# Kernel tuning notes

Hardware: AMD Instinct MI355X
Metric: run time of the kernel (lower is better)

The kernel has to match this reference:

```python
import jax, jax.numpy as jnp
import numpy as np

N, E, G, H, D = 30000, 480000, 128, 4, 64
NF, EF, GF, L = 92, 50, 108, 5
EPS = 1e-3  # keras BatchNormalization default epsilon


def _bn(t, g, b, m, v):
    # inference-mode batch norm with running stats
    return (t - m) * jax.lax.rsqrt(v + EPS) * g + b


def _forward(x, edge_attr, global_features,
             node_W, node_b, edge_W, edge_b,
             conv_W, conv_att, conv_bias, conv_bn_g, conv_bn_b, conv_bn_m, conv_bn_v,
             ga_W0, ga_b0, ga_bn0_g, ga_bn0_b, ga_bn0_m, ga_bn0_v,
             ga_W1, ga_b1, ga_bn1_g, ga_bn1_b, ga_bn1_m, ga_bn1_v,
             ga_W2, ga_b2, out_W0, out_b0, out_W1, out_b1,
             edge_index, batch_idx, num_graphs):
    lrelu = lambda t: jax.nn.leaky_relu(t, 0.2)
    row, col = edge_index[0], edge_index[1]
    n = x.shape[0]

    x = lrelu(x @ node_W + node_b)          # [N, D] node embedding
    ea = lrelu(edge_attr @ edge_W + edge_b)  # [E, D] edge embedding

    def conv(xc, p):
        W, att, bias, g, b, m, v = p
        xi = (jnp.concatenate([xc[row], ea], -1) @ W).reshape(-1, H, D)  # [E,H,D]
        xj = (jnp.concatenate([xc[col], ea], -1) @ W).reshape(-1, H, D)
        score = jnp.einsum('ehd,hd->eh', jnp.concatenate([xi, xj], -1), att)
        a = jnp.exp(_bn(lrelu(score), g, b, m, v))            # [E,H]
        norm = jax.ops.segment_sum(a, row, num_segments=n)    # edge softmax denom
        a = a / norm[row]
        msg = xj * a[..., None]                               # [E,H,D]
        # faithful to original: transpose then flat reshape before scatter-add
        msg = jnp.transpose(msg, (1, 0, 2)).reshape(-1, H * D)
        agg = jax.ops.segment_sum(msg, row, num_segments=n)
        out = agg.reshape(n, H, D).mean(axis=1) + bias
        return xc + out, None  # residual connection (done in GATGNN.call)

    x, _ = jax.lax.scan(conv, x, (conv_W, conv_att, conv_bias,
                                  conv_bn_g, conv_bn_b, conv_bn_m, conv_bn_v))

    # global attention pooling
    feat = jnp.concatenate([x, global_features[batch_idx]], -1)  # [N, D+GF]
    h = jax.nn.relu(_bn(feat @ ga_W0 + ga_b0, ga_bn0_g, ga_bn0_b, ga_bn0_m, ga_bn0_v))
    h = jax.nn.relu(_bn(h @ ga_W1 + ga_b1, ga_bn1_g, ga_bn1_b, ga_bn1_m, ga_bn1_v))
    a = jnp.exp(h @ ga_W2 + ga_b2)                               # [N,1]
    norm = jax.ops.segment_sum(a, batch_idx, num_segments=num_graphs)
    a = a / norm[batch_idx]
    pooled = jax.ops.segment_sum(x * a, batch_idx, num_segments=num_graphs)  # [G,D]
    out = jax.nn.relu(pooled @ out_W0 + out_b0) @ out_W1 + out_b1
    return out.squeeze(-1)  # output_dim == 1


def setup_inputs() -> dict:
    key = jax.random.key(0)
    ks = jax.random.split(key, 16)
    s = 0.05
    return {
        'x': jax.random.normal(ks[0], (N, NF), jnp.float32),
        'edge_attr': jax.random.normal(ks[1], (E, EF), jnp.float32),
        'global_features': jax.random.normal(ks[2], (G, GF), jnp.float32),
        'node_W': jax.random.normal(ks[3], (NF, D)) * s, 'node_b': jnp.zeros((D,)),
        'edge_W': jax.random.normal(ks[4], (EF, D)) * s, 'edge_b': jnp.zeros((D,)),
        'conv_W': jax.random.normal(ks[5], (L, 2 * D, H * D)) * s,
        'conv_att': jax.random.normal(ks[6], (L, H, 2 * D)) * s,
        'conv_bias': jnp.zeros((L, D)),
        'conv_bn_g': jnp.ones((L, H)), 'conv_bn_b': jnp.zeros((L, H)),
        'conv_bn_m': jnp.zeros((L, H)), 'conv_bn_v': jnp.ones((L, H)),
        'ga_W0': jax.random.normal(ks[7], (D + GF, D)) * s, 'ga_b0': jnp.zeros((D,)),
        'ga_bn0_g': jnp.ones((D,)), 'ga_bn0_b': jnp.zeros((D,)),
        'ga_bn0_m': jnp.zeros((D,)), 'ga_bn0_v': jnp.ones((D,)),
        'ga_W1': jax.random.normal(ks[8], (D, D)) * s, 'ga_b1': jnp.zeros((D,)),
        'ga_bn1_g': jnp.ones((D,)), 'ga_bn1_b': jnp.zeros((D,)),
        'ga_bn1_m': jnp.zeros((D,)), 'ga_bn1_v': jnp.ones((D,)),
        'ga_W2': jax.random.normal(ks[9], (D, 1)) * s, 'ga_b2': jnp.zeros((1,)),
        'out_W0': jax.random.normal(ks[10], (D, D)) * s, 'out_b0': jnp.zeros((D,)),
        'out_W1': jax.random.normal(ks[11], (D, 1)) * s, 'out_b1': jnp.zeros((1,)),
        'edge_index': jax.random.randint(ks[12], (2, E), 0, N),
        'batch_idx': jnp.sort(jax.random.randint(ks[13], (N,), 0, G)),
        'num_graphs': G,
    }


def reference(x, edge_attr, global_features, node_W, node_b, edge_W, edge_b,
              conv_W, conv_att, conv_bias, conv_bn_g, conv_bn_b, conv_bn_m, conv_bn_v,
              ga_W0, ga_b0, ga_bn0_g, ga_bn0_b, ga_bn0_m, ga_bn0_v,
              ga_W1, ga_b1, ga_bn1_g, ga_bn1_b, ga_bn1_m, ga_bn1_v,
              ga_W2, ga_b2, out_W0, out_b0, out_W1, out_b1,
              edge_index, batch_idx, num_graphs):
    return _forward(x, edge_attr, global_features, node_W, node_b, edge_W, edge_b,
                    conv_W, conv_att, conv_bias, conv_bn_g, conv_bn_b, conv_bn_m, conv_bn_v,
                    ga_W0, ga_b0, ga_bn0_g, ga_bn0_b, ga_bn0_m, ga_bn0_v,
                    ga_W1, ga_b1, ga_bn1_g, ga_bn1_b, ga_bn1_m, ga_bn1_v,
                    ga_W2, ga_b2, out_W0, out_b0, out_W1, out_b1,
                    edge_index, batch_idx, num_graphs)
```

## Files before the change

kernel.cpp:

```cpp
#include <hip/hip_runtime.h>

constexpr int N = 30000, E = 480000, G = 128, H = 4, D = 64;
constexpr int NF = 92, EF = 50, GF = 108, L = 5;
constexpr int EQ = E / 4;
constexpr float EPS = 1e-3f;

__device__ __forceinline__ float lrelu(float t) { return t > 0.f ? t : 0.2f * t; }

__device__ __forceinline__ unsigned short f2bf(float f) {
  unsigned int u = __float_as_uint(f);
  u += 0x7FFFu + ((u >> 16) & 1u);
  return (unsigned short)(u >> 16);
}
__device__ __forceinline__ float bf2f(unsigned short s) {
  return __uint_as_float(((unsigned int)s) << 16);
}

__global__ __launch_bounds__(256) void hist_kernel(const int* __restrict__ row,
                                                   int* __restrict__ deg) {
  int e = blockIdx.x * 256 + threadIdx.x;
  atomicAdd(&deg[row[e]], 1);
}

__global__ __launch_bounds__(1024) void scan_kernel(const int* __restrict__ deg,
                                                    int* __restrict__ start) {
  __shared__ int wsum[16];
  __shared__ int cbase;
  if (threadIdx.x == 0) cbase = 0;
  __syncthreads();
  int lane = threadIdx.x & 63, wave = threadIdx.x >> 6;
  for (int base = 0; base < N; base += 1024) {
    int i = base + (int)threadIdx.x;
    int v = (i < N) ? deg[i] : 0;
    int s = v;
#pragma unroll
    for (int off = 1; off < 64; off <<= 1) { int t = __shfl_up(s, off); if (lane >= off) s += t; }
    if (lane == 63) wsum[wave] = s;
    __syncthreads();
    if (wave == 0 && lane < 16) {
      int w = wsum[lane];
#pragma unroll
      for (int off = 1; off < 16; off <<= 1) { int t = __shfl_up(w, off); if (lane >= off) w += t; }
      wsum[lane] = w;
    }
    __syncthreads();
    int wbase = wave ? wsum[wave - 1] : 0;
    if (i < N) start[i] = cbase + wbase + (s - v);
    __syncthreads();
    if (threadIdx.x == 0) cbase += wsum[15];
    __syncthreads();
  }
  if (threadIdx.x == 0) start[N] = cbase;
}

__global__ __launch_bounds__(256) void fill_kernel(
    const int* __restrict__ row, const int* __restrict__ start, int* __restrict__ cur,
    int* __restrict__ eid_s) {
  int e = blockIdx.x * 256 + threadIdx.x;
  int r = row[e];
  int pos = start[r] + atomicAdd(&cur[r], 1);
  eid_s[pos] = e;
}

template <int K, bool BF16OUT>
__global__ __launch_bounds__(256) void embed7_kernel(
    const float* __restrict__ in, const float* __restrict__ W,
    const float* __restrict__ bias, float* __restrict__ outF,
    unsigned short* __restrict__ outB, int ntiles) {
  constexpr int KP = (K + 3) & ~3;
  constexpr int NL = (16 * K + 255) / 256;
  __shared__ float xs[2][16][KP];
  int tid = threadIdx.x, lane = tid & 63, wave = tid >> 6;
  if (K != KP) {
    for (int f = tid; f < 2 * 16 * KP; f += 256)
      if (f % KP >= K) ((float*)xs)[f] = 0.f;
  }
  float wreg[KP];
#pragma unroll
  for (int k = 0; k < K; k++) wreg[k] = W[k * 64 + lane];
#pragma unroll
  for (int k = K; k < KP; k++) wreg[k] = 0.f;
  float bb = bias[lane];
  float stage[NL];
  int t = blockIdx.x;
  if (t < ntiles) {
#pragma unroll
    for (int i = 0; i < NL; i++) { int f = tid + i * 256; if (f < 16 * K) stage[i] = in[(size_t)t * 16 * K + f]; }
#pragma unroll
    for (int i = 0; i < NL; i++) { int f = tid + i * 256; if (f < 16 * K) xs[0][f / K][f % K] = stage[i]; }
  }
  __syncthreads();
  int cur = 0;
  for (; t < ntiles; t += gridDim.x) {
    int nxt = t + gridDim.x;
    if (nxt < ntiles) {
#pragma unroll
      for (int i = 0; i < NL; i++) { int f = tid + i * 256; if (f < 16 * K) stage[i] = in[(size_t)nxt * 16 * K + f]; }
    }
    float a0 = 0.f, a1 = 0.f, a2 = 0.f, a3 = 0.f;
#pragma unroll
    for (int kc = 0; kc < KP / 4; kc++) {
      float4 x0 = *(const float4*)&xs[cur][wave * 4 + 0][kc * 4];
      float4 x1 = *(const float4*)&xs[cur][wave * 4 + 1][kc * 4];
      float4 x2 = *(const float4*)&xs[cur][wave * 4 + 2][kc * 4];
      float4 x3 = *(const float4*)&xs[cur][wave * 4 + 3][kc * 4];
      float w0 = wreg[kc * 4], w1 = wreg[kc * 4 + 1], w2 = wreg[kc * 4 + 2], w3 = wreg[kc * 4 + 3];
      a0 = fmaf(x0.x, w0, fmaf(x0.y, w1, fmaf(x0.z, w2, fmaf(x0.w, w3, a0))));
      a1 = fmaf(x1.x, w0, fmaf(x1.y, w1, fmaf(x1.z, w2, fmaf(x1.w, w3, a1))));
      a2 = fmaf(x2.x, w0, fmaf(x2.y, w1, fmaf(x2.z, w2, fmaf(x2.w, w3, a2))));
      a3 = fmaf(x3.x, w0, fmaf(x3.y, w1, fmaf(x3.z, w2, fmaf(x3.w, w3, a3))));
    }
    size_t o = ((size_t)t * 16 + wave * 4) * 64 + lane;
    float r0 = lrelu(a0 + bb), r1 = lrelu(a1 + bb), r2 = lrelu(a2 + bb), r3 = lrelu(a3 + bb);
    if (BF16OUT) {
      outB[o] = f2bf(r0); outB[o + 64] = f2bf(r1);
      outB[o + 128] = f2bf(r2); outB[o + 192] = f2bf(r3);
    } else {
      outF[o] = r0; outF[o + 64] = r1; outF[o + 128] = r2; outF[o + 192] = r3;
    }
    if (nxt < ntiles) {
#pragma unroll
      for (int i = 0; i < NL; i++) { int f = tid + i * 256; if (f < 16 * K) xs[cur ^ 1][f / K][f % K] = stage[i]; }
    }
    __syncthreads();
    cur ^= 1;
  }
}

__global__ __launch_bounds__(256) void aes_watt_all_kernel(
    const float* __restrict__ conv_W, const float* __restrict__ conv_att,
    float* __restrict__ AesT, float* __restrict__ WattT) {
  int l = blockIdx.x;
  const float* W = conv_W + (size_t)l * 128 * 256;
  const float* att = conv_att + (size_t)l * H * 128;
  int t = threadIdx.x;
  {
    int h = t >> 6, k = t & 63;
    float acc = 0.f;
    for (int d = 0; d < 64; d++)
      acc = fmaf(W[(64 + k) * 256 + h * 64 + d], att[h * 128 + d] + att[h * 128 + 64 + d], acc);
    AesT[l * 256 + h * 64 + k] = acc;
  }
  for (int idx = t; idx < 512; idx += 256) {
    int hh = idx >> 6, k = idx & 63;
    int h = hh >> 1, ij = hh & 1;
    float acc = 0.f;
    for (int d = 0; d < 64; d++)
      acc = fmaf(W[k * 256 + h * 64 + d], att[h * 128 + ij * 64 + d], acc);
    WattT[l * 512 + idx] = acc;
  }
}

__global__ __launch_bounds__(256) void qs_kernel(
    const unsigned short* __restrict__ ea, const float* __restrict__ AesT,
    float* __restrict__ qsAll) {
  int tid = threadIdx.x;
  int e = blockIdx.x * 16 + (tid >> 4);
  int k4 = tid & 15;
  uint2 raw = *(const uint2*)&ea[(size_t)e * 64 + k4 * 4];
  float e0 = __uint_as_float(raw.x << 16);
  float e1 = __uint_as_float(raw.x & 0xFFFF0000u);
  float e2 = __uint_as_float(raw.y << 16);
  float e3 = __uint_as_float(raw.y & 0xFFFF0000u);
#pragma unroll
  for (int l = 0; l < L; l++) {
    float q0, q1, q2, q3;
    {
      float4 c0 = *(const float4*)&AesT[l * 256 + 0 * 64 + k4 * 4];
      float4 c1 = *(const float4*)&AesT[l * 256 + 1 * 64 + k4 * 4];
      float4 c2 = *(const float4*)&AesT[l * 256 + 2 * 64 + k4 * 4];
      float4 c3 = *(const float4*)&AesT[l * 256 + 3 * 64 + k4 * 4];
      q0 = e0 * c0.x + e1 * c0.y + e2 * c0.z + e3 * c0.w;
      q1 = e0 * c1.x + e1 * c1.y + e2 * c1.z + e3 * c1.w;
      q2 = e0 * c2.x + e1 * c2.y + e2 * c2.z + e3 * c2.w;
      q3 = e0 * c3.x + e1 * c3.y + e2 * c3.z + e3 * c3.w;
    }
#pragma unroll
    for (int off = 1; off < 16; off <<= 1) {
      q0 += __shfl_xor(q0, off); q1 += __shfl_xor(q1, off);
      q2 += __shfl_xor(q2, off); q3 += __shfl_xor(q3, off);
    }
    if (k4 < 4) {
      float qv = (k4 == 0) ? q0 : (k4 == 1) ? q1 : (k4 == 2) ? q2 : q3;
      qsAll[(size_t)l * E * 4 + (size_t)e * 4 + k4] = qv;
    }
  }
}

__global__ __launch_bounds__(256) void xw_kernel(
    const float* __restrict__ xc, const float* __restrict__ W, const float* __restrict__ WattT,
    unsigned short* __restrict__ xWh, float* __restrict__ pi, float* __restrict__ pj) {
  __shared__ float xs[16][64];
  __shared__ float wlT[8][68];
  int tid = threadIdx.x, blk = blockIdx.x, n0 = blk * 16;
  for (int f = tid; f < 1024; f += 256) xs[f >> 6][f & 63] = xc[(size_t)n0 * 64 + f];
  for (int f = tid; f < 512; f += 256) wlT[f >> 6][f & 63] = WattT[f];
  __syncthreads();
  float acc[16];
#pragma unroll
  for (int n = 0; n < 16; n++) acc[n] = 0.f;
#pragma unroll 4
  for (int kc = 0; kc < 16; kc++) {
    float w0 = W[(4 * kc + 0) * 256 + tid];
    float w1 = W[(4 * kc + 1) * 256 + tid];
    float w2 = W[(4 * kc + 2) * 256 + tid];
    float w3 = W[(4 * kc + 3) * 256 + tid];
#pragma unroll
    for (int n = 0; n < 16; n++) {
      float4 xv = *(const float4*)&xs[n][4 * kc];
      acc[n] = fmaf(xv.x, w0, fmaf(xv.y, w1, fmaf(xv.z, w2, fmaf(xv.w, w3, acc[n]))));
    }
  }
  int h = tid >> 6, dd = tid & 63;
#pragma unroll
  for (int n = 0; n < 16; n++)
    xWh[((size_t)h * N + (n0 + n)) * 64 + dd] = f2bf(acc[n]);
  if (tid < 128) {
    int n = tid >> 3, hh = tid & 7;
    float a = 0.f;
#pragma unroll
    for (int kc = 0; kc < 16; kc++) {
      float4 xv = *(const float4*)&xs[n][4 * kc];
      float4 wv = *(const float4*)&wlT[hh][4 * kc];
      a = fmaf(xv.x, wv.x, fmaf(xv.y, wv.y, fmaf(xv.z, wv.z, fmaf(xv.w, wv.w, a))));
    }
    int hq = hh >> 1, ij = hh & 1;
    float* dst = ij ? pj : pi;
    dst[(n0 + n) * 4 + hq] = a;
  }
}

__global__ __launch_bounds__(256) void score2_kernel(
    const float* __restrict__ qs, const float* __restrict__ pi, const float* __restrict__ pj,
    const int* __restrict__ row, const int* __restrict__ col,
    const float* __restrict__ bng, const float* __restrict__ bnb,
    const float* __restrict__ bnm, const float* __restrict__ bnv,
    float* __restrict__ aArr) {
  int e = blockIdx.x * 256 + threadIdx.x;
  int r = row[e], c = col[e];
  float4 q = ((const float4*)qs)[e];
  float4 piv = ((const float4*)pi)[r];
  float4 pjv = ((const float4*)pj)[c];
  float A0 = bng[0] * rsqrtf(bnv[0] + EPS), B0 = bnb[0] - bnm[0] * A0;
  float A1 = bng[1] * rsqrtf(bnv[1] + EPS), B1 = bnb[1] - bnm[1] * A1;
  float A2 = bng[2] * rsqrtf(bnv[2] + EPS), B2 = bnb[2] - bnm[2] * A2;
  float A3 = bng[3] * rsqrtf(bnv[3] + EPS), B3 = bnb[3] - bnm[3] * A3;
  float4 out;
  out.x = expf(lrelu(piv.x + pjv.x + q.x) * A0 + B0);
  out.y = expf(lrelu(piv.y + pjv.y + q.y) * A1 + B1);
  out.z = expf(lrelu(piv.z + pjv.z + q.z) * A2 + B2);
  out.w = expf(lrelu(piv.w + pjv.w + q.w) * A3 + B3);
  ((float4*)aArr)[e] = out;
}

__global__ __launch_bounds__(256) void normsum_kernel(
    const float* __restrict__ aArr, const int* __restrict__ start,
    const int* __restrict__ eid_s, float* __restrict__ inv) {
  int n = blockIdx.x * 256 + threadIdx.x;
  if (n >= N) return;
  int s0 = start[n], s1 = start[n + 1];
  float4 s = {0.f, 0.f, 0.f, 0.f};
  int p = s0;
  for (; p + 4 <= s1; p += 4) {
    int e0 = eid_s[p], e1 = eid_s[p + 1], e2 = eid_s[p + 2], e3 = eid_s[p + 3];
    float4 a0 = ((const float4*)aArr)[e0];
    float4 a1 = ((const float4*)aArr)[e1];
    float4 a2 = ((const float4*)aArr)[e2];
    float4 a3 = ((const float4*)aArr)[e3];
    s.x += (a0.x + a1.x) + (a2.x + a3.x);
    s.y += (a0.y + a1.y) + (a2.y + a3.y);
    s.z += (a0.z + a1.z) + (a2.z + a3.z);
    s.w += (a0.w + a1.w) + (a2.w + a3.w);
  }
  for (; p < s1; p++) {
    float4 a = ((const float4*)aArr)[eid_s[p]];
    s.x += a.x; s.y += a.y; s.z += a.z; s.w += a.w;
  }
  float4 iv;
  if (s1 > s0) { iv.x = 1.f / s.x; iv.y = 1.f / s.y; iv.z = 1.f / s.z; iv.w = 1.f / s.w; }
  else         { iv.x = iv.y = iv.z = iv.w = 0.f; }
  ((float4*)inv)[n] = iv;
}

__global__ __launch_bounds__(256) void zyquad_kernel(
    const float* __restrict__ aArr, const float* __restrict__ invA,
    const unsigned short* __restrict__ ea, const unsigned short* __restrict__ xWh,
    const int* __restrict__ row, const int* __restrict__ col,
    unsigned short* __restrict__ Ybf, unsigned short* __restrict__ Zbf) {
  int q = blockIdx.x * 4 + (threadIdx.x >> 6);
  int lane = threadIdx.x & 63;
  const unsigned short* er = ea + (size_t)q * 256 + lane;
  float e0 = bf2f(er[0]), e1 = bf2f(er[64]), e2 = bf2f(er[128]), e3 = bf2f(er[192]);
  int4 rw = *(const int4*)&row[4 * q];
  int4 cl = *(const int4*)&col[4 * q];
  float4 A0 = ((const float4*)aArr)[4 * q + 0];
  float4 A1 = ((const float4*)aArr)[4 * q + 1];
  float4 A2 = ((const float4*)aArr)[4 * q + 2];
  float4 A3 = ((const float4*)aArr)[4 * q + 3];
  float4 I0 = ((const float4*)invA)[rw.x];
  float4 I1 = ((const float4*)invA)[rw.y];
  float4 I2 = ((const float4*)invA)[rw.z];
  float4 I3 = ((const float4*)invA)[rw.w];
  float c0[4] = {A0.x * I0.x, A0.y * I0.y, A0.z * I0.z, A0.w * I0.w};
  float c1[4] = {A1.x * I1.x, A1.y * I1.y, A1.z * I1.z, A1.w * I1.w};
  float c2[4] = {A2.x * I2.x, A2.y * I2.y, A2.z * I2.z, A2.w * I2.w};
  float c3[4] = {A3.x * I3.x, A3.y * I3.y, A3.z * I3.z, A3.w * I3.w};
#pragma unroll
  for (int h = 0; h < 4; h++) {
    const unsigned short* xw = xWh + (size_t)h * N * 64 + lane;
    float g0 = bf2f(xw[(size_t)cl.x * 64]);
    float g1 = bf2f(xw[(size_t)cl.y * 64]);
    float g2 = bf2f(xw[(size_t)cl.z * 64]);
    float g3 = bf2f(xw[(size_t)cl.w * 64]);
    float y = fmaf(c0[h], e0, fmaf(c1[h], e1, fmaf(c2[h], e2, c3[h] * e3)));
    float z = fmaf(c0[h], g0, fmaf(c1[h], g1, fmaf(c2[h], g2, c3[h] * g3)));
    size_t r = (size_t)h * EQ + q;
    Ybf[r * 64 + lane] = f2bf(y);
    Zbf[r * 64 + lane] = f2bf(z);
  }
}

__global__ __launch_bounds__(256) void scatter2_kernel(
    const unsigned short* __restrict__ Zbf, const unsigned short* __restrict__ Ybf,
    const int* __restrict__ start, const int* __restrict__ eid_s,
    float* __restrict__ out1, float* __restrict__ Bacc) {
  int wave = threadIdx.x >> 6, lane = threadIdx.x & 63;
  int n = blockIdx.x * 4 + wave;
  int s0 = __builtin_amdgcn_readfirstlane(start[n]);
  int s1 = __builtin_amdgcn_readfirstlane(start[n + 1]);
  float m = 0.f;
  float b0 = 0.f, b1 = 0.f, b2 = 0.f, b3 = 0.f;
  int p = s0;
  for (; p + 4 <= s1; p += 4) {
    int r0 = eid_s[p], r1 = eid_s[p + 1], r2 = eid_s[p + 2], r3 = eid_s[p + 3];
    float z0 = bf2f(Zbf[(size_t)r0 * 64 + lane]);
    float z1 = bf2f(Zbf[(size_t)r1 * 64 + lane]);
    float z2 = bf2f(Zbf[(size_t)r2 * 64 + lane]);
    float z3 = bf2f(Zbf[(size_t)r3 * 64 + lane]);
    float y0 = bf2f(Ybf[(size_t)r0 * 64 + lane]);
    float y1 = bf2f(Ybf[(size_t)r1 * 64 + lane]);
    float y2 = bf2f(Ybf[(size_t)r2 * 64 + lane]);
    float y3 = bf2f(Ybf[(size_t)r3 * 64 + lane]);
    m += (z0 + z1) + (z2 + z3);
    int h0 = r0 / EQ, h1 = r1 / EQ, h2 = r2 / EQ, h3 = r3 / EQ;
    if (h0 == 0) b0 += y0; else if (h0 == 1) b1 += y0; else if (h0 == 2) b2 += y0; else b3 += y0;
    if (h1 == 0) b0 += y1; else if (h1 == 1) b1 += y1; else if (h1 == 2) b2 += y1; else b3 += y1;
    if (h2 == 0) b0 += y2; else if (h2 == 1) b1 += y2; else if (h2 == 2) b2 += y2; else b3 += y2;
    if (h3 == 0) b0 += y3; else if (h3 == 1) b1 += y3; else if (h3 == 2) b2 += y3; else b3 += y3;
  }
  for (; p < s1; p++) {
    int r = eid_s[p];
    float z = bf2f(Zbf[(size_t)r * 64 + lane]);
    float y = bf2f(Ybf[(size_t)r * 64 + lane]);
    m += z;
    int h = r / EQ;
    if (h == 0) b0 += y; else if (h == 1) b1 += y; else if (h == 2) b2 += y; else b3 += y;
  }
  out1[(size_t)n * 64 + lane] = m;
  float* Bn = Bacc + (size_t)n * 256 + lane;
  Bn[0] = b0; Bn[64] = b1; Bn[128] = b2; Bn[192] = b3;
}

__global__ __launch_bounds__(256) void finish_kernel(
    const float* __restrict__ out1, const float* __restrict__ Bacc,
    const float* __restrict__ W, const float* __restrict__ bias, float* __restrict__ xc) {
  __shared__ float Bl[16][256];
  int tid = threadIdx.x, blk = blockIdx.x;
  for (int f = tid; f < 4096; f += 256) Bl[f >> 8][f & 255] = Bacc[(size_t)blk * 4096 + f];
  __syncthreads();
  int lane = tid & 63, wave = tid >> 6;
  float a0 = 0.f, a1 = 0.f, a2 = 0.f, a3 = 0.f;
#pragma unroll
  for (int h = 0; h < 4; h++) {
#pragma unroll 4
    for (int kc = 0; kc < 16; kc++) {
      float w0 = W[(64 + 4 * kc + 0) * 256 + h * 64 + lane];
      float w1 = W[(64 + 4 * kc + 1) * 256 + h * 64 + lane];
      float w2 = W[(64 + 4 * kc + 2) * 256 + h * 64 + lane];
      float w3 = W[(64 + 4 * kc + 3) * 256 + h * 64 + lane];
      float4 b0v = *(const float4*)&Bl[wave * 4 + 0][h * 64 + 4 * kc];
      float4 b1v = *(const float4*)&Bl[wave * 4 + 1][h * 64 + 4 * kc];
      float4 b2v = *(const float4*)&Bl[wave * 4 + 2][h * 64 + 4 * kc];
      float4 b3v = *(const float4*)&Bl[wave * 4 + 3][h * 64 + 4 * kc];
      a0 = fmaf(b0v.x, w0, fmaf(b0v.y, w1, fmaf(b0v.z, w2, fmaf(b0v.w, w3, a0))));
      a1 = fmaf(b1v.x, w0, fmaf(b1v.y, w1, fmaf(b1v.z, w2, fmaf(b1v.w, w3, a1))));
      a2 = fmaf(b2v.x, w0, fmaf(b2v.y, w1, fmaf(b2v.z, w2, fmaf(b2v.w, w3, a2))));
      a3 = fmaf(b3v.x, w0, fmaf(b3v.y, w1, fmaf(b3v.z, w2, fmaf(b3v.w, w3, a3))));
    }
  }
  float bb = bias[lane];
  size_t i0 = (size_t)(blk * 16 + wave * 4) * 64 + lane;
  xc[i0]       += bb + 0.25f * (out1[i0] + a0);
  xc[i0 + 64]  += bb + 0.25f * (out1[i0 + 64] + a1);
  xc[i0 + 128] += bb + 0.25f * (out1[i0 + 128] + a2);
  xc[i0 + 192] += bb + 0.25f * (out1[i0 + 192] + a3);
}

__global__ __launch_bounds__(256) void gacontrib_kernel(
    const float* __restrict__ gfeat, const float* __restrict__ W0,
    const float* __restrict__ b0, float* __restrict__ gc) {
  __shared__ float gs[16][GF];
  int tid = threadIdx.x, blk = blockIdx.x;
  int lane = tid & 63, wave = tid >> 6;
  for (int f = tid; f < 16 * GF; f += 256) gs[f / GF][f % GF] = gfeat[(size_t)blk * 16 * GF + f];
  float wreg[GF];
#pragma unroll
  for (int k = 0; k < GF; k++) wreg[k] = W0[(64 + k) * 64 + lane];
  __syncthreads();
  float a0 = 0.f, a1 = 0.f, a2 = 0.f, a3 = 0.f;
#pragma unroll
  for (int kc = 0; kc < GF / 4; kc++) {
    float4 x0 = *(const float4*)&gs[wave * 4 + 0][kc * 4];
    float4 x1 = *(const float4*)&gs[wave * 4 + 1][kc * 4];
    float4 x2 = *(const float4*)&gs[wave * 4 + 2][kc * 4];
    float4 x3 = *(const float4*)&gs[wave * 4 + 3][kc * 4];
    float w0 = wreg[kc * 4], w1 = wreg[kc * 4 + 1], w2 = wreg[kc * 4 + 2], w3 = wreg[kc * 4 + 3];
    a0 = fmaf(x0.x, w0, fmaf(x0.y, w1, fmaf(x0.z, w2, fmaf(x0.w, w3, a0))));
    a1 = fmaf(x1.x, w0, fmaf(x1.y, w1, fmaf(x1.z, w2, fmaf(x1.w, w3, a1))));
    a2 = fmaf(x2.x, w0, fmaf(x2.y, w1, fmaf(x2.z, w2, fmaf(x2.w, w3, a2))));
    a3 = fmaf(x3.x, w0, fmaf(x3.y, w1, fmaf(x3.z, w2, fmaf(x3.w, w3, a3))));
  }
  float bb = b0[lane];
  size_t o = ((size_t)blk * 16 + wave * 4) * 64 + lane;
  gc[o]       = a0 + bb;
  gc[o + 64]  = a1 + bb;
  gc[o + 128] = a2 + bb;
  gc[o + 192] = a3 + bb;
}

__global__ __launch_bounds__(256) void ga0_kernel(
    const float* __restrict__ xc, const float* __restrict__ gc, const int* __restrict__ batch,
    const float* __restrict__ W0,
    const float* __restrict__ g0, const float* __restrict__ bb0,
    const float* __restrict__ m0, const float* __restrict__ v0,
    float* __restrict__ hout, int ntiles) {
  __shared__ float xs[16][64];
  __shared__ int bl[16];
  int tid = threadIdx.x, lane = tid & 63, wave = tid >> 6;
  float wreg[64];
#pragma unroll
  for (int k = 0; k < 64; k++) wreg[k] = W0[k * 64 + lane];
  float sc = rsqrtf(v0[lane] + EPS) * g0[lane];
  float mm = m0[lane], be = bb0[lane];
  for (int t = blockIdx.x; t < ntiles; t += gridDim.x) {
    __syncthreads();
    if (tid < 16) bl[tid] = batch[t * 16 + tid];
    for (int f = tid; f < 1024; f += 256) xs[f >> 6][f & 63] = xc[(size_t)t * 1024 + f];
    __syncthreads();
    float a0 = 0.f, a1 = 0.f, a2 = 0.f, a3 = 0.f;
#pragma unroll
    for (int kc = 0; kc < 16; kc++) {
      float4 x0 = *(const float4*)&xs[wave * 4 + 0][kc * 4];
      float4 x1 = *(const float4*)&xs[wave * 4 + 1][kc * 4];
      float4 x2 = *(const float4*)&xs[wave * 4 + 2][kc * 4];
      float4 x3 = *(const float4*)&xs[wave * 4 + 3][kc * 4];
      float w0 = wreg[kc * 4], w1 = wreg[kc * 4 + 1], w2 = wreg[kc * 4 + 2], w3 = wreg[kc * 4 + 3];
      a0 = fmaf(x0.x, w0, fmaf(x0.y, w1, fmaf(x0.z, w2, fmaf(x0.w, w3, a0))));
      a1 = fmaf(x1.x, w0, fmaf(x1.y, w1, fmaf(x1.z, w2, fmaf(x1.w, w3, a1))));
      a2 = fmaf(x2.x, w0, fmaf(x2.y, w1, fmaf(x2.z, w2, fmaf(x2.w, w3, a2))));
      a3 = fmaf(x3.x, w0, fmaf(x3.y, w1, fmaf(x3.z, w2, fmaf(x3.w, w3, a3))));
    }
    a0 += gc[(size_t)bl[wave * 4 + 0] * 64 + lane];
    a1 += gc[(size_t)bl[wave * 4 + 1] * 64 + lane];
    a2 += gc[(size_t)bl[wave * 4 + 2] * 64 + lane];
    a3 += gc[(size_t)bl[wave * 4 + 3] * 64 + lane];
    size_t o = ((size_t)t * 16 + wave * 4) * 64 + lane;
    hout[o]       = fmaxf((a0 - mm) * sc + be, 0.f);
    hout[o + 64]  = fmaxf((a1 - mm) * sc + be, 0.f);
    hout[o + 128] = fmaxf((a2 - mm) * sc + be, 0.f);
    hout[o + 192] = fmaxf((a3 - mm) * sc + be, 0.f);
  }
}

__global__ __launch_bounds__(256) void ga1_kernel(
    const float* __restrict__ hbuf, const int* __restrict__ batch,
    const float* __restrict__ W1, const float* __restrict__ b1,
    const float* __restrict__ g1, const float* __restrict__ bb1,
    const float* __restrict__ m1, const float* __restrict__ v1,
    const float* __restrict__ W2, const float* __restrict__ b2,
    float* __restrict__ a_un, float* __restrict__ norm_g, int ntiles) {
  __shared__ float hsh[16][64];
  __shared__ int bl[16];
  int tid = threadIdx.x, lane = tid & 63, wave = tid >> 6;
  float wreg[64];
#pragma unroll
  for (int k = 0; k < 64; k++) wreg[k] = W1[k * 64 + lane];
  float sc1 = rsqrtf(v1[lane] + EPS) * g1[lane];
  float mm1 = m1[lane], be1 = bb1[lane], bb1v = b1[lane];
  float w2v = W2[lane], b2v = b2[0];
  for (int t = blockIdx.x; t < ntiles; t += gridDim.x) {
    __syncthreads();
    if (tid < 16) bl[tid] = batch[t * 16 + tid];
    for (int f = tid; f < 1024; f += 256) hsh[f >> 6][f & 63] = hbuf[(size_t)t * 1024 + f];
    __syncthreads();
    float c0 = 0.f, c1 = 0.f, c2 = 0.f, c3 = 0.f;
#pragma unroll
    for (int kc = 0; kc < 16; kc++) {
      float4 x0 = *(const float4*)&hsh[wave * 4 + 0][kc * 4];
      float4 x1 = *(const float4*)&hsh[wave * 4 + 1][kc * 4];
      float4 x2 = *(const float4*)&hsh[wave * 4 + 2][kc * 4];
      float4 x3 = *(const float4*)&hsh[wave * 4 + 3][kc * 4];
      float w0 = wreg[kc * 4], w1 = wreg[kc * 4 + 1], w2 = wreg[kc * 4 + 2], w3 = wreg[kc * 4 + 3];
      c0 = fmaf(x0.x, w0, fmaf(x0.y, w1, fmaf(x0.z, w2, fmaf(x0.w, w3, c0))));
      c1 = fmaf(x1.x, w0, fmaf(x1.y, w1, fmaf(x1.z, w2, fmaf(x1.w, w3, c1))));
      c2 = fmaf(x2.x, w0, fmaf(x2.y, w1, fmaf(x2.z, w2, fmaf(x2.w, w3, c2))));
      c3 = fmaf(x3.x, w0, fmaf(x3.y, w1, fmaf(x3.z, w2, fmaf(x3.w, w3, c3))));
    }
    float p0 = fmaxf((c0 + bb1v - mm1) * sc1 + be1, 0.f) * w2v;
    float p1 = fmaxf((c1 + bb1v - mm1) * sc1 + be1, 0.f) * w2v;
    float p2 = fmaxf((c2 + bb1v - mm1) * sc1 + be1, 0.f) * w2v;
    float p3 = fmaxf((c3 + bb1v - mm1) * sc1 + be1, 0.f) * w2v;
#pragma unroll
    for (int off = 1; off < 64; off <<= 1) {
      p0 += __shfl_xor(p0, off); p1 += __shfl_xor(p1, off);
      p2 += __shfl_xor(p2, off); p3 += __shfl_xor(p3, off);
    }
    if (lane < 4) {
      float pv = (lane == 0) ? p0 : (lane == 1) ? p1 : (lane == 2) ? p2 : p3;
      float a = expf(pv + b2v);
      int node = t * 16 + wave * 4 + lane;
      a_un[node] = a;
      atomicAdd(&norm_g[bl[wave * 4 + lane]], a);
    }
  }
}

__global__ __launch_bounds__(256) void pool_kernel(
    const float* __restrict__ xc, const float* __restrict__ a_un,
    const float* __restrict__ norm_g, const int* __restrict__ batch,
    float* __restrict__ pooled) {
  int n = blockIdx.x * 4 + (threadIdx.x >> 6);
  int d = threadIdx.x & 63;
  int b = batch[n];
  float coef = a_un[n] / norm_g[b];
  atomicAdd(&pooled[b * 64 + d], xc[(size_t)n * 64 + d] * coef);
}

__global__ __launch_bounds__(256) void final_kernel(
    const float* __restrict__ pooled, const float* __restrict__ W0,
    const float* __restrict__ b0, const float* __restrict__ W1,
    const float* __restrict__ b1, float* __restrict__ out) {
  int g = blockIdx.x * 4 + (threadIdx.x >> 6);
  int d = threadIdx.x & 63;
  float pv = pooled[g * 64 + d];
  float acc = b0[d];
  for (int k = 0; k < 64; k++) acc = fmaf(__shfl(pv, k), W0[k * 64 + d], acc);
  acc = fmaxf(acc, 0.f);
  float p = acc * W1[d];
  for (int off = 1; off < 64; off <<= 1) p += __shfl_xor(p, off);
  if (d == 0) out[g] = p + b1[0];
}

extern "C" void kernel_launch(void* const* d_in, const int* in_sizes, int n_in,
                              void* d_out, int out_size, void* d_ws, size_t ws_size,
                              hipStream_t stream) {
  (void)in_sizes; (void)n_in; (void)out_size; (void)ws_size;
  const float* x_in    = (const float*)d_in[0];
  const float* ea_in   = (const float*)d_in[1];
  const float* gf      = (const float*)d_in[2];
  const float* node_W  = (const float*)d_in[3];
  const float* node_b  = (const float*)d_in[4];
  const float* edge_W  = (const float*)d_in[5];
  const float* edge_b  = (const float*)d_in[6];
  const float* conv_W  = (const float*)d_in[7];
  const float* conv_att= (const float*)d_in[8];
  const float* conv_bias=(const float*)d_in[9];
  const float* bn_g = (const float*)d_in[10];
  const float* bn_b = (const float*)d_in[11];
  const float* bn_m = (const float*)d_in[12];
  const float* bn_v = (const float*)d_in[13];
  const float* ga_W0 = (const float*)d_in[14]; const float* ga_b0 = (const float*)d_in[15];
  const float* ga0g = (const float*)d_in[16];  const float* ga0b = (const float*)d_in[17];
  const float* ga0m = (const float*)d_in[18];  const float* ga0v = (const float*)d_in[19];
  const float* ga_W1 = (const float*)d_in[20]; const float* ga_b1 = (const float*)d_in[21];
  const float* ga1g = (const float*)d_in[22];  const float* ga1b = (const float*)d_in[23];
  const float* ga1m = (const float*)d_in[24];  const float* ga1v = (const float*)d_in[25];
  const float* ga_W2 = (const float*)d_in[26]; const float* ga_b2 = (const float*)d_in[27];
  const float* out_W0 = (const float*)d_in[28]; const float* out_b0 = (const float*)d_in[29];
  const float* out_W1 = (const float*)d_in[30]; const float* out_b1 = (const float*)d_in[31];
  const int* eidx  = (const int*)d_in[32];
  const int* row   = eidx;
  const int* col   = eidx + E;
  const int* batch = (const int*)d_in[33];

  float* ws = (float*)d_ws;
  size_t off = 0;
  auto alloc = [&](size_t n) { float* p = ws + off; off += (n + 63) & ~(size_t)63; return p; };
  float* x_cur  = alloc((size_t)N * D);
  unsigned short* ea_bf = (unsigned short*)alloc((size_t)E * 32);
  unsigned short* xWh   = (unsigned short*)alloc((size_t)N * 128);
  unsigned short* Ybf   = (unsigned short*)alloc((size_t)E * 32);
  unsigned short* Zbf   = (unsigned short*)alloc((size_t)E * 32);
  float* pi     = alloc((size_t)N * 4);
  float* pj     = alloc((size_t)N * 4);
  float* aArr   = alloc((size_t)E * 4);
  float* invA   = alloc((size_t)N * 4);
  float* out1   = alloc((size_t)N * 64);
  float* Bacc   = alloc((size_t)N * 256);
  float* AesT   = alloc(L * 256);
  float* WattT  = alloc(L * 512);
  float* a_un   = alloc(N);
  float* norm_g = alloc(G);
  float* pooled = alloc((size_t)G * 64);
  int* start = (int*)alloc(N + 1);
  int* eid_s = (int*)alloc(E);
  float* qsAll  = alloc((size_t)L * E * 4);
  int* deg = (int*)xWh;
  int* cur = deg + N;
  float* gcontrib = (float*)xWh;
  float* hbuf     = Bacc;

  hipMemsetAsync(deg, 0, (size_t)2 * N * sizeof(int), stream);
  hist_kernel<<<E / 256, 256, 0, stream>>>(row, deg);
  scan_kernel<<<1, 1024, 0, stream>>>(deg, start);
  fill_kernel<<<E / 256, 256, 0, stream>>>(row, start, cur, eid_s);

  embed7_kernel<NF, false><<<960, 256, 0, stream>>>(x_in, node_W, node_b, x_cur, nullptr, N / 16);
  embed7_kernel<EF, true><<<1920, 256, 0, stream>>>(ea_in, edge_W, edge_b, nullptr, ea_bf, E / 16);

  aes_watt_all_kernel<<<L, 256, 0, stream>>>(conv_W, conv_att, AesT, WattT);
  qs_kernel<<<E / 16, 256, 0, stream>>>(ea_bf, AesT, qsAll);

  for (int l = 0; l < L; l++) {
    const float* W = conv_W + (size_t)l * 128 * 256;
    xw_kernel<<<N / 16, 256, 0, stream>>>(x_cur, W, WattT + l * 512, xWh, pi, pj);
    score2_kernel<<<E / 256, 256, 0, stream>>>(qsAll + (size_t)l * E * 4, pi, pj, row, col,
                                               bn_g + l * H, bn_b + l * H,
                                               bn_m + l * H, bn_v + l * H, aArr);
    normsum_kernel<<<(N + 255) / 256, 256, 0, stream>>>(aArr, start, eid_s, invA);
    zyquad_kernel<<<EQ / 4, 256, 0, stream>>>(aArr, invA, ea_bf, xWh, row, col, Ybf, Zbf);
    scatter2_kernel<<<N / 4, 256, 0, stream>>>(Zbf, Ybf, start, eid_s, out1, Bacc);
    finish_kernel<<<N / 16, 256, 0, stream>>>(out1, Bacc, W, conv_bias + l * D, x_cur);
  }

  hipMemsetAsync(norm_g, 0, G * sizeof(float), stream);
  hipMemsetAsync(pooled, 0, (size_t)G * 64 * sizeof(float), stream);
  gacontrib_kernel<<<G / 16, 256, 0, stream>>>(gf, ga_W0, ga_b0, gcontrib);
  ga0_kernel<<<960, 256, 0, stream>>>(x_cur, gcontrib, batch, ga_W0,
                                      ga0g, ga0b, ga0m, ga0v, hbuf, N / 16);
  ga1_kernel<<<960, 256, 0, stream>>>(hbuf, batch, ga_W1, ga_b1,
                                      ga1g, ga1b, ga1m, ga1v, ga_W2, ga_b2,
                                      a_un, norm_g, N / 16);
  pool_kernel<<<N / 4, 256, 0, stream>>>(x_cur, a_un, norm_g, batch, pooled);
  final_kernel<<<G / 4, 256, 0, stream>>>(pooled, out_W0, out_b0, out_W1, out_b1,
                                          (float*)d_out);
}
```

Baseline: 1.383 ms.

## Replace atomic graph pooling with segment-bounded per-graph reduction

Computes per-graph node ranges from the sorted batch index, then pools with one block per graph that sums the attention normaliser and the weighted features locally. This removes the atomicAdd on norm_g in ga1, the per-element atomic scatter in the old pool kernel, and two memsets. It adds a small boundary kernel and relies on batch_idx being sorted. Only 128 blocks are launched, so a large graph serialises within one block.

```diff
diff --git a/kernel.cpp b/kernel.cpp
--- a/kernel.cpp
+++ b/kernel.cpp
@@ -60,6 +60,16 @@
   int r = row[e];
   int pos = start[r] + atomicAdd(&cur[r], 1);
   eid_s[pos] = e;
+}
+
+__global__ __launch_bounds__(256) void gbound_kernel(const int* __restrict__ batch,
+                                                     int* __restrict__ gstart) {
+  int n = blockIdx.x * 256 + threadIdx.x;
+  if (n >= N) return;
+  int b = batch[n];
+  int prev = (n == 0) ? -1 : batch[n - 1];
+  for (int g = prev + 1; g <= b; g++) gstart[g] = n;
+  if (n == N - 1) for (int g = b + 1; g <= G; g++) gstart[g] = N;
 }
 
 template <int K, bool BF16OUT>
@@ -473,14 +483,13 @@
 }
 
 __global__ __launch_bounds__(256) void ga1_kernel(
-    const float* __restrict__ hbuf, const int* __restrict__ batch,
+    const float* __restrict__ hbuf,
     const float* __restrict__ W1, const float* __restrict__ b1,
     const float* __restrict__ g1, const float* __restrict__ bb1,
     const float* __restrict__ m1, const float* __restrict__ v1,
     const float* __restrict__ W2, const float* __restrict__ b2,
-    float* __restrict__ a_un, float* __restrict__ norm_g, int ntiles) {
+    float* __restrict__ a_un, int ntiles) {
   __shared__ float hsh[16][64];
-  __shared__ int bl[16];
   int tid = threadIdx.x, lane = tid & 63, wave = tid >> 6;
   float wreg[64];
 #pragma unroll
@@ -490,7 +499,6 @@
   float w2v = W2[lane], b2v = b2[0];
   for (int t = blockIdx.x; t < ntiles; t += gridDim.x) {
     __syncthreads();
-    if (tid < 16) bl[tid] = batch[t * 16 + tid];
     for (int f = tid; f < 1024; f += 256) hsh[f >> 6][f & 63] = hbuf[(size_t)t * 1024 + f];
     __syncthreads();
     float c0 = 0.f, c1 = 0.f, c2 = 0.f, c3 = 0.f;
@@ -517,23 +525,37 @@
     }
     if (lane < 4) {
       float pv = (lane == 0) ? p0 : (lane == 1) ? p1 : (lane == 2) ? p2 : p3;
-      float a = expf(pv + b2v);
-      int node = t * 16 + wave * 4 + lane;
-      a_un[node] = a;
-      atomicAdd(&norm_g[bl[wave * 4 + lane]], a);
-    }
-  }
-}
-
-__global__ __launch_bounds__(256) void pool_kernel(
+      a_un[t * 16 + wave * 4 + lane] = expf(pv + b2v);
+    }
+  }
+}
+
+__global__ __launch_bounds__(256) void pool2_kernel(
     const float* __restrict__ xc, const float* __restrict__ a_un,
-    const float* __restrict__ norm_g, const int* __restrict__ batch,
-    float* __restrict__ pooled) {
-  int n = blockIdx.x * 4 + (threadIdx.x >> 6);
-  int d = threadIdx.x & 63;
-  int b = batch[n];
-  float coef = a_un[n] / norm_g[b];
-  atomicAdd(&pooled[b * 64 + d], xc[(size_t)n * 64 + d] * coef);
+    const int* __restrict__ gstart, float* __restrict__ pooled) {
+  __shared__ float red[4][64];
+  __shared__ float s_norm;
+  int g = blockIdx.x;
+  int tid = threadIdx.x, lane = tid & 63, wave = tid >> 6;
+  int s0 = gstart[g], s1 = gstart[g + 1];
+  float ns = 0.f;
+  for (int n = s0 + tid; n < s1; n += 256) ns += a_un[n];
+#pragma unroll
+  for (int off = 1; off < 64; off <<= 1) ns += __shfl_xor(ns, off);
+  if (lane == 0) red[wave][0] = ns;
+  __syncthreads();
+  if (tid == 0) s_norm = (red[0][0] + red[1][0]) + (red[2][0] + red[3][0]);
+  __syncthreads();
+  float inv = (s1 > s0) ? 1.f / s_norm : 0.f;
+  __syncthreads();
+  float acc = 0.f;
+  for (int n = s0 + wave; n < s1; n += 4)
+    acc = fmaf(xc[(size_t)n * 64 + lane], a_un[n], acc);
+  red[wave][lane] = acc;
+  __syncthreads();
+  if (wave == 0)
+    pooled[(size_t)g * 64 + lane] =
+        inv * ((red[0][lane] + red[1][lane]) + (red[2][lane] + red[3][lane]));
 }
 
 __global__ __launch_bounds__(256) void final_kernel(
@@ -600,9 +622,9 @@
   float* AesT   = alloc(L * 256);
   float* WattT  = alloc(L * 512);
   float* a_un   = alloc(N);
-  float* norm_g = alloc(G);
   float* pooled = alloc((size_t)G * 64);
   int* start = (int*)alloc(N + 1);
+  int* gstart = (int*)alloc(G + 1);
   int* eid_s = (int*)alloc(E);
   float* qsAll  = alloc((size_t)L * E * 4);
   int* deg = (int*)xWh;
@@ -614,6 +636,7 @@
   hist_kernel<<<E / 256, 256, 0, stream>>>(row, deg);
   scan_kernel<<<1, 1024, 0, stream>>>(deg, start);
   fill_kernel<<<E / 256, 256, 0, stream>>>(row, start, cur, eid_s);
+  gbound_kernel<<<(N + 255) / 256, 256, 0, stream>>>(batch, gstart);
 
   embed7_kernel<NF, false><<<960, 256, 0, stream>>>(x_in, node_W, node_b, x_cur, nullptr, N / 16);
   embed7_kernel<EF, true><<<1920, 256, 0, stream>>>(ea_in, edge_W, edge_b, nullptr, ea_bf, E / 16);
@@ -633,15 +656,13 @@
     finish_kernel<<<N / 16, 256, 0, stream>>>(out1, Bacc, W, conv_bias + l * D, x_cur);
   }
 
-  hipMemsetAsync(norm_g, 0, G * sizeof(float), stream);
-  hipMemsetAsync(pooled, 0, (size_t)G * 64 * sizeof(float), stream);
   gacontrib_kernel<<<G / 16, 256, 0, stream>>>(gf, ga_W0, ga_b0, gcontrib);
   ga0_kernel<<<960, 256, 0, stream>>>(x_cur, gcontrib, batch, ga_W0,
                                       ga0g, ga0b, ga0m, ga0v, hbuf, N / 16);
-  ga1_kernel<<<960, 256, 0, stream>>>(hbuf, batch, ga_W1, ga_b1,
+  ga1_kernel<<<960, 256, 0, stream>>>(hbuf, ga_W1, ga_b1,
                                       ga1g, ga1b, ga1m, ga1v, ga_W2, ga_b2,
-                                      a_un, norm_g, N / 16);
-  pool_kernel<<<N / 4, 256, 0, stream>>>(x_cur, a_un, norm_g, batch, pooled);
+                                      a_un, N / 16);
+  pool2_kernel<<<G, 256, 0, stream>>>(x_cur, a_un, gstart, pooled);
   final_kernel<<<G / 4, 256, 0, stream>>>(pooled, out_W0, out_b0, out_W1, out_b1,
                                           (float*)d_out);
 }
```

New measurement: 1.257 ms. -9.1%, faster.
